# Kernel optimization log

Hardware: AMD Instinct MI355X
Metric: run time of the kernel (lower is better)

## Reference

```python
import jax, jax.numpy as jnp
import numpy as np

SCALE = 100.0

def square_distance(src, dst):
    # src: [B,N,D], dst: [B,M,D] -> [B,N,M] squared euclidean distances
    d = -2.0 * jnp.einsum('bnd,bmd->bnm', src, dst)
    d = d + jnp.sum(src * src, axis=-1)[:, :, None]
    d = d + jnp.sum(dst * dst, axis=-1)[:, None, :]
    return d

def setup_inputs() -> dict:
    key = jax.random.key(0)
    k1, k2 = jax.random.split(key)
    B, N, M, D = 8, 8192, 8192, 3
    pred = jax.random.normal(k1, (B, N, D), dtype=jnp.float32)
    gt = jax.random.normal(k2, (B, M, D), dtype=jnp.float32)
    return {"pred": pred, "gt": gt}

def reference(pred, gt):
    dis = square_distance(pred, gt)              # [B,N,M]
    pred_to_gt = jnp.min(dis, axis=2).mean(axis=1)  # [B]
    gt_to_pred = jnp.min(dis, axis=1).mean(axis=1)  # [B]
    return (0.5 * pred_to_gt + 0.5 * gt_to_pred).mean() * SCALE
```

## Files before the change

kernel.cpp:

```cpp
#include <hip/hip_runtime.h>


#define B_DIM 8
#define N_DIM 8192
#define MT    (N_DIM / 32)
#define CH    16
#define NC    (MT / CH)
#define BLOCK 256
#define PPW   2

typedef short  bf16x8 __attribute__((ext_vector_type(8)));
typedef float  f32x16 __attribute__((ext_vector_type(16)));

__device__ __forceinline__ unsigned short bf16_rne(float f) {
    unsigned int u = __float_as_uint(f);
    u += 0x7fffu + ((u >> 16) & 1u);
    return (unsigned short)(u >> 16);
}
__device__ __forceinline__ float bf16f(unsigned short h) {
    return __uint_as_float(((unsigned int)h) << 16);
}

__global__ __launch_bounds__(256) void chamfer_prep(
    const float* __restrict__ pred, const float* __restrict__ gt,
    unsigned short* __restrict__ bpack, float* __restrict__ out)
{
    const int i   = blockIdx.x * 256 + threadIdx.x;
    if (i == 0) out[0] = 0.0f;
    const int dir = i >> 16;
    const int bm  = i & 0xFFFF;
    const float* dst = dir ? pred : gt;
    const float x = dst[3*bm+0], y = dst[3*bm+1], z = dst[3*bm+2];
    const unsigned short hx = bf16_rne(x), hy = bf16_rne(y), hz = bf16_rne(z);
    const unsigned short lx = bf16_rne(x - bf16f(hx));
    const unsigned short ly = bf16_rne(y - bf16f(hy));
    const unsigned short lz = bf16_rne(z - bf16f(hz));
    const float gn = x*x + y*y + z*z;
    const unsigned short gnh = bf16_rne(gn), gnl = bf16_rne(gn - bf16f(gnh));
    const unsigned short one = 0x3F80;

    const int b  = bm >> 13, m = bm & (N_DIM - 1);
    const int mt = m >> 5,   c = m & 31;
    const int dirb = (dir << 3) | b;
    unsigned short* p0 = bpack + ((size_t)(dirb * MT + mt) * 64 + c) * 8;
    unsigned short* p1 = p0 + 32 * 8;
    bf16x8 h0 = {(short)hx,(short)hy,(short)hz,(short)lx,(short)ly,(short)lz,(short)hx,(short)hy};
    bf16x8 h1 = {(short)hz,(short)one,(short)one,(short)gnh,(short)gnl,0,0,0};
    *(bf16x8*)p0 = h0;
    *(bf16x8*)p1 = h1;
}

__global__ __launch_bounds__(BLOCK, 2) void chamfer_partial(
    const float* __restrict__ pred, const float* __restrict__ gt,
    const bf16x8* __restrict__ bpack, float* __restrict__ out)
{
    __shared__ bf16x8 sbuf[2][CH * 64];
    __shared__ float wsum[4];
    const int dirb = blockIdx.x;
    const int dir  = dirb >> 3, b = dirb & 7;
    const int w    = threadIdx.x >> 6, lane = threadIdx.x & 63;
    const int half = lane >> 5,  col = lane & 31;

    const float* src  = dir ? gt : pred;
    const float* srcb = src + (size_t)b * N_DIM * 3;

    bf16x8 afrag[PPW];
    #pragma unroll
    for (int p = 0; p < PPW; ++p) {
        const int ntile = (blockIdx.y * 4 + w) * PPW + p;
        const int n = ntile * 32 + col;
        const float x = srcb[3*n+0], y = srcb[3*n+1], z = srcb[3*n+2];
        const float ax = -2.f*x, ay = -2.f*y, az = -2.f*z;
        const unsigned short ahx = bf16_rne(ax), ahy = bf16_rne(ay), ahz = bf16_rne(az);
        const unsigned short alx = bf16_rne(ax - bf16f(ahx));
        const unsigned short aly = bf16_rne(ay - bf16f(ahy));
        const unsigned short alz = bf16_rne(az - bf16f(ahz));
        const float pn = x*x + y*y + z*z;
        const unsigned short pnh = bf16_rne(pn), pnl = bf16_rne(pn - bf16f(pnh));
        const unsigned short one = 0x3F80;
        bf16x8 a0 = {(short)ahx,(short)ahy,(short)ahz,(short)ahx,(short)ahy,(short)ahz,(short)alx,(short)aly};
        bf16x8 a1 = {(short)alz,(short)pnh,(short)pnl,(short)one,(short)one,0,0,0};
        afrag[p] = (half == 0) ? a0 : a1;
    }

    const bf16x8* bp = bpack + (size_t)dirb * MT * 64;
    const f32x16 czero = {0.f,0.f,0.f,0.f,0.f,0.f,0.f,0.f,
                          0.f,0.f,0.f,0.f,0.f,0.f,0.f,0.f};
    float best[PPW][16];
    #pragma unroll
    for (int p = 0; p < PPW; ++p)
        #pragma unroll
        for (int r = 0; r < 16; ++r) best[p][r] = 1e30f;

    bf16x8 rg[4];
    const int soff = w * 256 + lane;
    #define GLOAD(c) { const bf16x8* g = bp + (size_t)(c) * (CH*64) + soff; \
        _Pragma("unroll") for (int i = 0; i < 4; ++i) rg[i] = g[i * 64]; }
    #define SWRITE(pb) { bf16x8* s = &sbuf[pb][soff]; \
        _Pragma("unroll") for (int i = 0; i < 4; ++i) s[i * 64] = rg[i]; }

    GLOAD(0); SWRITE(0); GLOAD(1);
    __syncthreads();

    for (int c = 0; c < NC; ++c) {
        const int pb = c & 1;
        if (c + 1 < NC) SWRITE(pb ^ 1);
        if (c + 2 < NC) GLOAD(c + 2);
        #pragma unroll 8
        for (int j = 0; j < CH; ++j) {
            const bf16x8 bc = sbuf[pb][j * 64 + lane];
            #pragma unroll
            for (int p = 0; p < PPW; ++p) {
                f32x16 d = __builtin_amdgcn_mfma_f32_32x32x16_bf16(afrag[p], bc, czero, 0, 0, 0);
                #pragma unroll
                for (int r = 0; r < 16; ++r) best[p][r] = fminf(best[p][r], d[r]);
            }
        }
        __syncthreads();
    }

    float bsum = 0.f;
    #pragma unroll
    for (int p = 0; p < PPW; ++p) {
        float s = 0.f;
        #pragma unroll
        for (int r = 0; r < 16; ++r) {
            float v = best[p][r];
            v = fminf(v, __shfl_xor(v, 1,  64));
            v = fminf(v, __shfl_xor(v, 2,  64));
            v = fminf(v, __shfl_xor(v, 4,  64));
            v = fminf(v, __shfl_xor(v, 8,  64));
            v = fminf(v, __shfl_xor(v, 16, 64));
            s += v;
        }
        bsum += s + __shfl_xor(s, 32, 64);
    }
    if (lane == 0) wsum[w] = bsum;
    __syncthreads();
    if (threadIdx.x == 0) {
        const float scale = 100.0f * 0.5f / ((float)B_DIM * (float)N_DIM);
        atomicAdd(out, (wsum[0] + wsum[1] + wsum[2] + wsum[3]) * scale);
    }
}

extern "C" void kernel_launch(void* const* d_in, const int* in_sizes, int n_in,
                              void* d_out, int out_size, void* d_ws, size_t ws_size,
                              hipStream_t stream) {
    const float* pred = (const float*)d_in[0];
    const float* gt   = (const float*)d_in[1];
    float* out = (float*)d_out;
    unsigned short* bpack = (unsigned short*)d_ws;

    chamfer_prep<<<(2 * B_DIM * N_DIM) / 256, 256, 0, stream>>>(pred, gt, bpack, out);

    dim3 grid(16, N_DIM / (32 * 4 * PPW));
    chamfer_partial<<<grid, BLOCK, 0, stream>>>(pred, gt, (const bf16x8*)bpack, out);
}
```

Before: 94.27 us.

## Split M dimension across blocks with atomicMin keys and async global-to-LDS loads

Splits the inner M loop across two blocks per row tile, so the grid doubles. Per-row minima are merged through ordered-uint atomicMin into a workspace key array, and a third kernel sums them. Staging now uses global_load_lds direct-to-LDS copies in place of register round-trips, the MFMA inner loop is paired, and occupancy bounds are raised to 4. The cost is an extra kernel launch, extra atomics and extra workspace traffic in exchange for more parallelism and less register pressure.

After: 100.3 us. 6.4% more time.

```diff
diff --git a/kernel.cpp b/kernel.cpp
--- a/kernel.cpp
+++ b/kernel.cpp
@@ -4,8 +4,10 @@
 #define B_DIM 8
 #define N_DIM 8192
 #define MT    (N_DIM / 32)
+#define MSPLIT 2
+#define MTB   (MT / MSPLIT)
 #define CH    16
-#define NC    (MT / CH)
+#define NC    (MTB / CH)
 #define BLOCK 256
 #define PPW   2
 
@@ -20,13 +22,22 @@
 __device__ __forceinline__ float bf16f(unsigned short h) {
     return __uint_as_float(((unsigned int)h) << 16);
 }
+__device__ __forceinline__ unsigned int f32_to_ordered_u32(float f) {
+    unsigned int u = __float_as_uint(f);
+    return (u & 0x80000000u) ? ~u : (u | 0x80000000u);
+}
+__device__ __forceinline__ float ordered_u32_to_f32(unsigned int k) {
+    return __uint_as_float((k & 0x80000000u) ? (k & 0x7fffffffu) : ~k);
+}
 
 __global__ __launch_bounds__(256) void chamfer_prep(
     const float* __restrict__ pred, const float* __restrict__ gt,
-    unsigned short* __restrict__ bpack, float* __restrict__ out)
+    unsigned short* __restrict__ bpack, unsigned int* __restrict__ keys,
+    float* __restrict__ out)
 {
     const int i   = blockIdx.x * 256 + threadIdx.x;
     if (i == 0) out[0] = 0.0f;
+    keys[i] = 0xFFFFFFFFu;
     const int dir = i >> 16;
     const int bm  = i & 0xFFFF;
     const float* dst = dir ? pred : gt;
@@ -50,25 +61,26 @@
     *(bf16x8*)p1 = h1;
 }
 
-__global__ __launch_bounds__(BLOCK, 2) void chamfer_partial(
+__global__ __launch_bounds__(BLOCK, 4) void chamfer_partial(
     const float* __restrict__ pred, const float* __restrict__ gt,
-    const bf16x8* __restrict__ bpack, float* __restrict__ out)
+    const bf16x8* __restrict__ bpack, unsigned int* __restrict__ keys)
 {
     __shared__ bf16x8 sbuf[2][CH * 64];
-    __shared__ float wsum[4];
     const int dirb = blockIdx.x;
     const int dir  = dirb >> 3, b = dirb & 7;
     const int w    = threadIdx.x >> 6, lane = threadIdx.x & 63;
     const int half = lane >> 5,  col = lane & 31;
+    const int ms   = blockIdx.z;
 
     const float* src  = dir ? gt : pred;
     const float* srcb = src + (size_t)b * N_DIM * 3;
 
     bf16x8 afrag[PPW];
+    int ntile[PPW];
     #pragma unroll
     for (int p = 0; p < PPW; ++p) {
-        const int ntile = (blockIdx.y * 4 + w) * PPW + p;
-        const int n = ntile * 32 + col;
+        ntile[p] = (blockIdx.y * 4 + w) * PPW + p;
+        const int n = ntile[p] * 32 + col;
         const float x = srcb[3*n+0], y = srcb[3*n+1], z = srcb[3*n+2];
         const float ax = -2.f*x, ay = -2.f*y, az = -2.f*z;
         const unsigned short ahx = bf16_rne(ax), ahy = bf16_rne(ay), ahz = bf16_rne(az);
@@ -83,7 +95,7 @@
         afrag[p] = (half == 0) ? a0 : a1;
     }
 
-    const bf16x8* bp = bpack + (size_t)dirb * MT * 64;
+    const bf16x8* bp = bpack + (size_t)dirb * MT * 64 + (size_t)ms * MTB * 64;
     const f32x16 czero = {0.f,0.f,0.f,0.f,0.f,0.f,0.f,0.f,
                           0.f,0.f,0.f,0.f,0.f,0.f,0.f,0.f};
     float best[PPW][16];
@@ -92,37 +104,40 @@
         #pragma unroll
         for (int r = 0; r < 16; ++r) best[p][r] = 1e30f;
 
-    bf16x8 rg[4];
-    const int soff = w * 256 + lane;
-    #define GLOAD(c) { const bf16x8* g = bp + (size_t)(c) * (CH*64) + soff; \
-        _Pragma("unroll") for (int i = 0; i < 4; ++i) rg[i] = g[i * 64]; }
-    #define SWRITE(pb) { bf16x8* s = &sbuf[pb][soff]; \
-        _Pragma("unroll") for (int i = 0; i < 4; ++i) s[i * 64] = rg[i]; }
+    #define GLL(c, pb) { \
+        _Pragma("unroll") for (int i = 0; i < 4; ++i) { \
+            const bf16x8* g = bp + (size_t)(c) * (CH*64) + w*256 + i*64 + lane; \
+            __builtin_amdgcn_global_load_lds( \
+                (const __attribute__((address_space(1))) void*)g, \
+                (__attribute__((address_space(3))) void*)&sbuf[pb][w*256 + i*64], \
+                16, 0, 0); \
+        } }
 
-    GLOAD(0); SWRITE(0); GLOAD(1);
+    GLL(0, 0);
     __syncthreads();
 
     for (int c = 0; c < NC; ++c) {
         const int pb = c & 1;
-        if (c + 1 < NC) SWRITE(pb ^ 1);
-        if (c + 2 < NC) GLOAD(c + 2);
-        #pragma unroll 8
-        for (int j = 0; j < CH; ++j) {
-            const bf16x8 bc = sbuf[pb][j * 64 + lane];
+        if (c + 1 < NC) GLL(c + 1, pb ^ 1);
+        #pragma unroll
+        for (int j = 0; j < CH; j += 2) {
+            const bf16x8 b0 = sbuf[pb][(j  ) * 64 + lane];
+            const bf16x8 b1 = sbuf[pb][(j+1) * 64 + lane];
             #pragma unroll
             for (int p = 0; p < PPW; ++p) {
-                f32x16 d = __builtin_amdgcn_mfma_f32_32x32x16_bf16(afrag[p], bc, czero, 0, 0, 0);
+                f32x16 d0 = __builtin_amdgcn_mfma_f32_32x32x16_bf16(afrag[p], b0, czero, 0, 0, 0);
+                f32x16 d1 = __builtin_amdgcn_mfma_f32_32x32x16_bf16(afrag[p], b1, czero, 0, 0, 0);
                 #pragma unroll
-                for (int r = 0; r < 16; ++r) best[p][r] = fminf(best[p][r], d[r]);
+                for (int r = 0; r < 16; ++r)
+                    best[p][r] = fminf(fminf(best[p][r], d0[r]), d1[r]);
             }
         }
         __syncthreads();
     }
 
-    float bsum = 0.f;
+    unsigned int* kb = keys + (size_t)dirb * N_DIM;
     #pragma unroll
     for (int p = 0; p < PPW; ++p) {
-        float s = 0.f;
         #pragma unroll
         for (int r = 0; r < 16; ++r) {
             float v = best[p][r];
@@ -131,16 +146,27 @@
             v = fminf(v, __shfl_xor(v, 4,  64));
             v = fminf(v, __shfl_xor(v, 8,  64));
             v = fminf(v, __shfl_xor(v, 16, 64));
-            s += v;
+            const int row = (r & 3) + 8 * (r >> 2) + 4 * half;
+            if (col == r)
+                atomicMin(&kb[ntile[p] * 32 + row], f32_to_ordered_u32(v));
         }
-        bsum += s + __shfl_xor(s, 32, 64);
     }
-    if (lane == 0) wsum[w] = bsum;
+}
+
+__global__ __launch_bounds__(256) void chamfer_reduce(
+    const unsigned int* __restrict__ keys, float* __restrict__ out)
+{
+    const float scale = 100.0f * 0.5f / ((float)B_DIM * (float)N_DIM);
+    const int i = (blockIdx.x * 256 + threadIdx.x) * 4;
+    const uint4 k = *(const uint4*)(keys + i);
+    float s = ordered_u32_to_f32(k.x) + ordered_u32_to_f32(k.y)
+            + ordered_u32_to_f32(k.z) + ordered_u32_to_f32(k.w);
+    for (int off = 32; off > 0; off >>= 1) s += __shfl_down(s, off, 64);
+    __shared__ float wsum[4];
+    if ((threadIdx.x & 63) == 0) wsum[threadIdx.x >> 6] = s;
     __syncthreads();
-    if (threadIdx.x == 0) {
-        const float scale = 100.0f * 0.5f / ((float)B_DIM * (float)N_DIM);
+    if (threadIdx.x == 0)
         atomicAdd(out, (wsum[0] + wsum[1] + wsum[2] + wsum[3]) * scale);
-    }
 }
 
 extern "C" void kernel_launch(void* const* d_in, const int* in_sizes, int n_in,
@@ -150,9 +176,12 @@
     const float* gt   = (const float*)d_in[1];
     float* out = (float*)d_out;
     unsigned short* bpack = (unsigned short*)d_ws;
+    unsigned int* keys = (unsigned int*)((char*)d_ws + (size_t)16 * MT * 64 * 16);
 
-    chamfer_prep<<<(2 * B_DIM * N_DIM) / 256, 256, 0, stream>>>(pred, gt, bpack, out);
+    chamfer_prep<<<(2 * B_DIM * N_DIM) / 256, 256, 0, stream>>>(pred, gt, bpack, keys, out);
 
-    dim3 grid(16, N_DIM / (32 * 4 * PPW));
-    chamfer_partial<<<grid, BLOCK, 0, stream>>>(pred, gt, (const bf16x8*)bpack, out);
+    dim3 grid(16, N_DIM / (32 * 4 * PPW), MSPLIT);
+    chamfer_partial<<<grid, BLOCK, 0, stream>>>(pred, gt, (const bf16x8*)bpack, keys);
+
+    chamfer_reduce<<<(2 * B_DIM * N_DIM) / (256 * 4), 256, 0, stream>>>(keys, out);
 }
```
